# Performance work log

Hardware: AMD Instinct MI355X
Metric: run time of the kernel (lower is better)

Reference implementation:

```python
import jax, jax.numpy as jnp
import numpy as np

N, F, M, E = 8192, 256, 128, 131072


def setup_inputs() -> dict:
    key = jax.random.key(0)
    k = jax.random.split(key, 6)
    x = jax.random.normal(k[0], (N, F), dtype=jnp.float32)
    edge_index = jax.random.randint(k[1], (2, E), 0, N, dtype=jnp.int64)
    eps = jax.random.normal(k[2], (N, M), dtype=jnp.float32)
    # small init scale so sigmoid(z_i . z_j) isn't saturated
    W_mu = jax.random.normal(k[3], (F, M), dtype=jnp.float32) * 0.05
    b_mu = jnp.zeros((M,), dtype=jnp.float32)
    W_sig = jax.random.normal(k[4], (F, M), dtype=jnp.float32) * 0.05
    b_sig = jnp.zeros((M,), dtype=jnp.float32)
    return {"x": x, "edge_index": edge_index, "eps": eps,
            "W_mu": W_mu, "b_mu": b_mu, "W_sig": W_sig, "b_sig": b_sig}


def reference(x, edge_index, eps, W_mu, b_mu, W_sig, b_sig):
    # Gaussian encoder: Normal(mu, exp(logstd)), Independent over latent dim
    mu = x @ W_mu + b_mu                      # [N, M]
    logstd = x @ W_sig + b_sig                # [N, M]
    sigma = jnp.exp(logstd)
    z = mu + sigma * eps                      # rsample, [N, M]

    # decoder.probability(dot(z_i, z_j)) = sigmoid(logit); vectorized as Z @ Z.T
    logits = z @ z.T                          # [N, N]

    # symmetric adjacency labels from edge_index (either direction counts)
    src, dst = edge_index[0], edge_index[1]
    adj = jnp.zeros((N, N), dtype=jnp.float32)
    adj = adj.at[src, dst].set(1.0)
    adj = adj.at[dst, src].set(1.0)

    # BCE(sigmoid(s), y) summed over unordered pairs i < j (stable logits form)
    per_pair = jax.nn.softplus(logits) - adj * logits  # = -[y log p + (1-y) log(1-p)]
    triu = jnp.triu(jnp.ones((N, N), dtype=bool), k=1)
    bce = jnp.sum(jnp.where(triu, per_pair, 0.0))

    # sum_i KL( N(mu_i, sigma_i) || N(0, I) )
    kl = jnp.sum(0.5 * (sigma * sigma + mu * mu - 1.0) - logstd)

    return bce + 0.001 * kl
```

## Files before the change

### kernel.cpp

```cpp
#include <hip/hip_runtime.h>

#define NN 8192
#define FF 256
#define MM 128
#define HSLOTS 262144
#define NTILES 2080

typedef __attribute__((ext_vector_type(8))) short bf16x8;
typedef __attribute__((ext_vector_type(4))) float f32x4;

#define P_KL    0
#define P_EDGE  (64 * 16)
#define P_SP    (128 * 16)
#define Z_OFF   16384
#define Z_BYTES (NN * MM * 2)
#define HASH_OFF (Z_OFF + Z_BYTES)
#define WT_OFF  (HASH_OFF + HSLOTS * 4)
#define WT_BYTES (MM * FF * 2)

__device__ __forceinline__ float wave_reduce(float v) {
    #pragma unroll
    for (int off = 32; off > 0; off >>= 1) v += __shfl_down(v, off);
    return v;
}
__device__ __forceinline__ unsigned short f2bf(float f) {
    unsigned int u = __float_as_uint(f);
    u += 0x7fffu + ((u >> 16) & 1u);
    return (unsigned short)(u >> 16);
}
__device__ __forceinline__ int4 pack8(float4 a, float4 b) {
    int4 p;
    p.x = (int)f2bf(a.x) | ((int)f2bf(a.y) << 16);
    p.y = (int)f2bf(a.z) | ((int)f2bf(a.w) << 16);
    p.z = (int)f2bf(b.x) | ((int)f2bf(b.y) << 16);
    p.w = (int)f2bf(b.z) | ((int)f2bf(b.w) << 16);
    return p;
}

__global__ __launch_bounds__(256)
void prep_w(const float* __restrict__ Wmu, const float* __restrict__ Wsg,
            unsigned short* __restrict__ WmuT, unsigned short* __restrict__ WsgT,
            float* __restrict__ part, unsigned int* __restrict__ ht) {
    const int t = blockIdx.x * 256 + threadIdx.x;
    const int n = t >> 8, f = t & 255;
    WmuT[t] = f2bf(Wmu[f * MM + n]);
    WsgT[t] = f2bf(Wsg[f * MM + n]);
    if (t < 4096) part[t] = 0.f;
    uint4 z4 = {0u, 0u, 0u, 0u};
    ((uint4*)ht)[t * 2]     = z4;
    ((uint4*)ht)[t * 2 + 1] = z4;
}

#define XP_I4 33
#define XP_S  264

__global__ __launch_bounds__(256)
void encoder_mfma(const float* __restrict__ x, const float* __restrict__ eps,
                  const unsigned short* __restrict__ WmuT,
                  const unsigned short* __restrict__ WsgT,
                  const float* __restrict__ bmu, const float* __restrict__ bsg,
                  unsigned short* __restrict__ zb, float* __restrict__ part) {
    __shared__ int4 ax[16 * XP_I4];
    __shared__ float red[4];
    const int tid = threadIdx.x;
    const int wid = tid >> 6, lane = tid & 63;
    const int l15 = lane & 15, quad = lane >> 4;
    const int row0 = blockIdx.x * 16;

    {
        const int r = tid >> 4, ch = tid & 15;
        const float4* g0 = (const float4*)(x + (size_t)(row0 + r) * FF + ch * 8);
        const float4* g1 = (const float4*)(x + (size_t)(row0 + r) * FF + (ch + 16) * 8);
        ax[r * XP_I4 + ch]      = pack8(g0[0], g0[1]);
        ax[r * XP_I4 + ch + 16] = pack8(g1[0], g1[1]);
    }
    __syncthreads();

    const short* sax = (const short*)ax;
    const int4* wtm = (const int4*)WmuT;
    const int4* wts = (const int4*)WsgT;

    f32x4 zero4 = {0.f, 0.f, 0.f, 0.f};
    f32x4 accm[2], accl[2];
    accm[0] = accm[1] = accl[0] = accl[1] = zero4;

    #pragma unroll
    for (int ks = 0; ks < 8; ++ks) {
        const bf16x8 a = *(const bf16x8*)&sax[l15 * XP_S + ks * 32 + quad * 8];
        #pragma unroll
        for (int j = 0; j < 2; ++j) {
            const int n = wid * 32 + j * 16 + l15;
            const bf16x8 bmf = *(const bf16x8*)&wtm[n * 32 + ks * 4 + quad];
            const bf16x8 bsf = *(const bf16x8*)&wts[n * 32 + ks * 4 + quad];
            accm[j] = __builtin_amdgcn_mfma_f32_16x16x32_bf16(a, bmf, accm[j], 0, 0, 0);
            accl[j] = __builtin_amdgcn_mfma_f32_16x16x32_bf16(a, bsf, accl[j], 0, 0, 0);
        }
    }

    float klp = 0.f;
    #pragma unroll
    for (int j = 0; j < 2; ++j) {
        const int col = wid * 32 + j * 16 + l15;
        const float bm = bmu[col], bs = bsg[col];
        #pragma unroll
        for (int r = 0; r < 4; ++r) {
            const int row = row0 + quad * 4 + r;
            const float mu = accm[j][r] + bm;
            const float ls = accl[j][r] + bs;
            const float sg = __expf(ls);
            const float zz = fmaf(sg, eps[(size_t)row * MM + col], mu);
            zb[(size_t)row * MM + col] = f2bf(zz);
            klp += 0.5f * (sg * sg + mu * mu - 1.f) - ls;
        }
    }

    klp = wave_reduce(klp);
    if (lane == 0) red[wid] = klp;
    __syncthreads();
    if (tid == 0)
        atomicAdd(&part[P_KL + (blockIdx.x & 63) * 16],
                  red[0] + red[1] + red[2] + red[3]);
}

__device__ __forceinline__ float dotpair(unsigned int a, unsigned int b) {
    const float al = __uint_as_float(a << 16);
    const float ah = __uint_as_float(a & 0xffff0000u);
    const float bl = __uint_as_float(b << 16);
    const float bh = __uint_as_float(b & 0xffff0000u);
    return fmaf(al, bl, ah * bh);
}

__global__ __launch_bounds__(256, 3)
void tile_edge_kernel(const unsigned short* __restrict__ zb,
                      const int* __restrict__ ei, int E,
                      unsigned int* __restrict__ ht,
                      float* __restrict__ part) {
    __shared__ int4 la[128 * 8];
    __shared__ int4 lb[128 * 8];

    const int tid = threadIdx.x;
    const int bid = blockIdx.x;

    int bi = (int)((129.0f - sqrtf(16641.0f - 8.0f * (float)bid)) * 0.5f);
    bi = min(max(bi, 0), 63);
    while ((bi * (129 - bi)) / 2 > bid) --bi;
    while (((bi + 1) * (128 - bi)) / 2 <= bid) ++bi;
    const int bj = bi + (bid - (bi * (129 - bi)) / 2);

    const int wid = tid >> 6, lane = tid & 63;
    const int wm = wid >> 1, wn = wid & 1;
    const int l15 = lane & 15, quad = lane >> 4;
    const int xk = l15 & 7;

    const int4* ga = (const int4*)(zb + (size_t)bi * 128 * MM);
    const int4* gb = (const int4*)(zb + (size_t)bj * 128 * MM);

    f32x4 zero4 = {0.f, 0.f, 0.f, 0.f};
    f32x4 acc[4][4];
    #pragma unroll
    for (int i = 0; i < 4; ++i)
        #pragma unroll
        for (int j = 0; j < 4; ++j) acc[i][j] = zero4;

    const short* sa = (const short*)la;
    const short* sb = (const short*)lb;

    #pragma unroll
    for (int kc = 0; kc < 2; ++kc) {
        if (kc) __syncthreads();
        #pragma unroll
        for (int i = 0; i < 4; ++i) {
            const int c = tid + i * 256;
            const int row = c >> 3, ch = c & 7;
            const int sl = ch ^ (row & 7);
            la[row * 8 + sl] = ga[row * 16 + kc * 8 + ch];
            lb[row * 8 + sl] = gb[row * 16 + kc * 8 + ch];
        }
        __syncthreads();
        #pragma unroll
        for (int ks = 0; ks < 2; ++ks) {
            const int kq = ks * 4 + quad;
            bf16x8 af[4], bfr[4];
            #pragma unroll
            for (int t2 = 0; t2 < 4; ++t2) {
                const int ar = wm * 64 + t2 * 16 + l15;
                af[t2]  = *(const bf16x8*)&sa[ar * 64 + ((kq ^ xk) * 8)];
                const int br = wn * 64 + t2 * 16 + l15;
                bfr[t2] = *(const bf16x8*)&sb[br * 64 + ((kq ^ xk) * 8)];
            }
            #pragma unroll
            for (int i = 0; i < 4; ++i)
                #pragma unroll
                for (int j = 0; j < 4; ++j)
                    acc[i][j] = __builtin_amdgcn_mfma_f32_16x16x32_bf16(
                        af[i], bfr[j], acc[i][j], 0, 0, 0);
        }
    }

    float tsum = 0.f;
    if (bi != bj) {
        #pragma unroll
        for (int i = 0; i < 4; ++i)
            #pragma unroll
            for (int j = 0; j < 4; ++j)
                #pragma unroll
                for (int r = 0; r < 4; ++r) {
                    const float v = acc[i][j][r];
                    const float e = __expf(-fabsf(v));
                    tsum += fmaxf(v, 0.f) + e * fmaf(e, -0.5f, 1.f);
                }
    } else {
        const int rbase = wm * 64 + quad * 4;
        const int cbase = wn * 64 + l15;
        #pragma unroll
        for (int i = 0; i < 4; ++i)
            #pragma unroll
            for (int j = 0; j < 4; ++j)
                #pragma unroll
                for (int r = 0; r < 4; ++r)
                    if (cbase + j * 16 > rbase + i * 16 + r) {
                        const float v = acc[i][j][r];
                        const float e = __expf(-fabsf(v));
                        tsum += fmaxf(v, 0.f) + e * fmaf(e, -0.5f, 1.f);
                    }
    }

    tsum = wave_reduce(tsum);
    if (lane == 0)
        atomicAdd(&part[P_SP + ((bi * 64 + bj + wid * 16) & 63) * 16], tsum);

    if (bid < (E >> 6) && wid == (bid & 3)) {
        const int e = bid * 64 + lane;
        float contrib = 0.f;
        const int i = ei[e];
        const int j = ei[E + e];
        if (i != j) {
            const int a = min(i, j), b = max(i, j);
            const uint4* za = (const uint4*)(zb + (size_t)a * MM);
            const uint4* zc = (const uint4*)(zb + (size_t)b * MM);
            float s = 0.f;
            #pragma unroll
            for (int q = 0; q < MM / 8; ++q) {
                const uint4 ua = za[q], ub = zc[q];
                s += dotpair(ua.x, ub.x) + dotpair(ua.y, ub.y)
                   + dotpair(ua.z, ub.z) + dotpair(ua.w, ub.w);
            }
            const unsigned int key = (unsigned int)a * NN + b;
            unsigned int slot = (key * 2654435761u) & (HSLOTS - 1);
            bool first = false;
            for (;;) {
                const unsigned int old = atomicCAS(&ht[slot], 0u, key);
                if (old == 0u) { first = true; break; }
                if (old == key) break;
                slot = (slot + 1) & (HSLOTS - 1);
            }
            if (first) contrib = s;
        }
        contrib = wave_reduce(contrib);
        if (lane == 0)
            atomicAdd(&part[P_EDGE + (bid & 63) * 16], contrib);
    }
}

__global__ void combine_kernel(const float* __restrict__ part,
                               float* __restrict__ out) {
    const int t = threadIdx.x;
    float v = part[P_SP + t * 16] - part[P_EDGE + t * 16]
            + 0.001f * part[P_KL + t * 16];
    v = wave_reduce(v);
    if (t == 0) out[0] = v;
}

extern "C" void kernel_launch(void* const* d_in, const int* in_sizes, int n_in,
                              void* d_out, int out_size, void* d_ws, size_t ws_size,
                              hipStream_t stream) {
    const float* x   = (const float*)d_in[0];
    const int* ei    = (const int*)d_in[1];
    const float* eps = (const float*)d_in[2];
    const float* Wmu = (const float*)d_in[3];
    const float* bmu = (const float*)d_in[4];
    const float* Wsg = (const float*)d_in[5];
    const float* bsg = (const float*)d_in[6];
    float* out = (float*)d_out;
    char* ws = (char*)d_ws;

    float* part = (float*)ws;
    unsigned short* zb = (unsigned short*)(ws + Z_OFF);
    unsigned int* ht = (unsigned int*)(ws + HASH_OFF);
    unsigned short* WmuT = (unsigned short*)(ws + WT_OFF);
    unsigned short* WsgT = (unsigned short*)(ws + WT_OFF + WT_BYTES);
    const int E = in_sizes[1] / 2;

    prep_w<<<128, 256, 0, stream>>>(Wmu, Wsg, WmuT, WsgT, part, ht);
    encoder_mfma<<<NN / 16, 256, 0, stream>>>(x, eps, WmuT, WsgT, bmu, bsg, zb, part);
    tile_edge_kernel<<<NTILES, 256, 0, stream>>>(zb, ei, E, ht, part);
    combine_kernel<<<1, 64, 0, stream>>>(part, out);
}
```

Before: 119.7 us.

## Fuse all four kernels into one persistent cooperative kernel with grid syncs

Replaces the four separate launches (weight prep, encoder, tile/edge, combine) with one cooperative persistent kernel that loops over work units and uses grid-wide syncs between phases. The edge-label work is now spread across waves in reverse block order, so it runs alongside the tile work instead of being tied to the first tile blocks. This is meant to remove launch gaps and per-kernel tail effects. In exchange it adds grid.sync barriers, limits the grid to the occupancy-derived resident count, and calls an occupancy query on the host on every launch.

```diff
diff --git a/kernel.cpp b/kernel.cpp
--- a/kernel.cpp
+++ b/kernel.cpp
@@ -1,4 +1,7 @@
 #include <hip/hip_runtime.h>
+#include <hip/hip_cooperative_groups.h>
+
+namespace cg = cooperative_groups;
 
 #define NN 8192
 #define FF 256
@@ -17,6 +20,8 @@
 #define HASH_OFF (Z_OFF + Z_BYTES)
 #define WT_OFF  (HASH_OFF + HSLOTS * 4)
 #define WT_BYTES (MM * FF * 2)
+#define XP_I4 33
+#define XP_S  264
 
 __device__ __forceinline__ float wave_reduce(float v) {
     #pragma unroll
@@ -36,92 +41,6 @@
     p.w = (int)f2bf(b.z) | ((int)f2bf(b.w) << 16);
     return p;
 }
-
-__global__ __launch_bounds__(256)
-void prep_w(const float* __restrict__ Wmu, const float* __restrict__ Wsg,
-            unsigned short* __restrict__ WmuT, unsigned short* __restrict__ WsgT,
-            float* __restrict__ part, unsigned int* __restrict__ ht) {
-    const int t = blockIdx.x * 256 + threadIdx.x;
-    const int n = t >> 8, f = t & 255;
-    WmuT[t] = f2bf(Wmu[f * MM + n]);
-    WsgT[t] = f2bf(Wsg[f * MM + n]);
-    if (t < 4096) part[t] = 0.f;
-    uint4 z4 = {0u, 0u, 0u, 0u};
-    ((uint4*)ht)[t * 2]     = z4;
-    ((uint4*)ht)[t * 2 + 1] = z4;
-}
-
-#define XP_I4 33
-#define XP_S  264
-
-__global__ __launch_bounds__(256)
-void encoder_mfma(const float* __restrict__ x, const float* __restrict__ eps,
-                  const unsigned short* __restrict__ WmuT,
-                  const unsigned short* __restrict__ WsgT,
-                  const float* __restrict__ bmu, const float* __restrict__ bsg,
-                  unsigned short* __restrict__ zb, float* __restrict__ part) {
-    __shared__ int4 ax[16 * XP_I4];
-    __shared__ float red[4];
-    const int tid = threadIdx.x;
-    const int wid = tid >> 6, lane = tid & 63;
-    const int l15 = lane & 15, quad = lane >> 4;
-    const int row0 = blockIdx.x * 16;
-
-    {
-        const int r = tid >> 4, ch = tid & 15;
-        const float4* g0 = (const float4*)(x + (size_t)(row0 + r) * FF + ch * 8);
-        const float4* g1 = (const float4*)(x + (size_t)(row0 + r) * FF + (ch + 16) * 8);
-        ax[r * XP_I4 + ch]      = pack8(g0[0], g0[1]);
-        ax[r * XP_I4 + ch + 16] = pack8(g1[0], g1[1]);
-    }
-    __syncthreads();
-
-    const short* sax = (const short*)ax;
-    const int4* wtm = (const int4*)WmuT;
-    const int4* wts = (const int4*)WsgT;
-
-    f32x4 zero4 = {0.f, 0.f, 0.f, 0.f};
-    f32x4 accm[2], accl[2];
-    accm[0] = accm[1] = accl[0] = accl[1] = zero4;
-
-    #pragma unroll
-    for (int ks = 0; ks < 8; ++ks) {
-        const bf16x8 a = *(const bf16x8*)&sax[l15 * XP_S + ks * 32 + quad * 8];
-        #pragma unroll
-        for (int j = 0; j < 2; ++j) {
-            const int n = wid * 32 + j * 16 + l15;
-            const bf16x8 bmf = *(const bf16x8*)&wtm[n * 32 + ks * 4 + quad];
-            const bf16x8 bsf = *(const bf16x8*)&wts[n * 32 + ks * 4 + quad];
-            accm[j] = __builtin_amdgcn_mfma_f32_16x16x32_bf16(a, bmf, accm[j], 0, 0, 0);
-            accl[j] = __builtin_amdgcn_mfma_f32_16x16x32_bf16(a, bsf, accl[j], 0, 0, 0);
-        }
-    }
-
-    float klp = 0.f;
-    #pragma unroll
-    for (int j = 0; j < 2; ++j) {
-        const int col = wid * 32 + j * 16 + l15;
-        const float bm = bmu[col], bs = bsg[col];
-        #pragma unroll
-        for (int r = 0; r < 4; ++r) {
-            const int row = row0 + quad * 4 + r;
-            const float mu = accm[j][r] + bm;
-            const float ls = accl[j][r] + bs;
-            const float sg = __expf(ls);
-            const float zz = fmaf(sg, eps[(size_t)row * MM + col], mu);
-            zb[(size_t)row * MM + col] = f2bf(zz);
-            klp += 0.5f * (sg * sg + mu * mu - 1.f) - ls;
-        }
-    }
-
-    klp = wave_reduce(klp);
-    if (lane == 0) red[wid] = klp;
-    __syncthreads();
-    if (tid == 0)
-        atomicAdd(&part[P_KL + (blockIdx.x & 63) * 16],
-                  red[0] + red[1] + red[2] + red[3]);
-}
-
 __device__ __forceinline__ float dotpair(unsigned int a, unsigned int b) {
     const float al = __uint_as_float(a << 16);
     const float ah = __uint_as_float(a & 0xffff0000u);
@@ -129,146 +48,232 @@
     const float bh = __uint_as_float(b & 0xffff0000u);
     return fmaf(al, bl, ah * bh);
 }
+__device__ __forceinline__ float aload(const float* p) {
+    return __hip_atomic_load(p, __ATOMIC_RELAXED, __HIP_MEMORY_SCOPE_AGENT);
+}
 
 __global__ __launch_bounds__(256, 3)
-void tile_edge_kernel(const unsigned short* __restrict__ zb,
-                      const int* __restrict__ ei, int E,
-                      unsigned int* __restrict__ ht,
-                      float* __restrict__ part) {
+void mega_kernel(const float* __restrict__ x, const float* __restrict__ eps,
+                 const float* __restrict__ Wmu, const float* __restrict__ Wsg,
+                 const float* __restrict__ bmu, const float* __restrict__ bsg,
+                 const int* __restrict__ ei, int E,
+                 unsigned short* __restrict__ WmuT,
+                 unsigned short* __restrict__ WsgT,
+                 unsigned short* __restrict__ zb,
+                 unsigned int* __restrict__ ht,
+                 float* __restrict__ part, float* __restrict__ out) {
     __shared__ int4 la[128 * 8];
     __shared__ int4 lb[128 * 8];
-
+    __shared__ float red[4];
+
+    cg::grid_group grid = cg::this_grid();
     const int tid = threadIdx.x;
     const int bid = blockIdx.x;
-
-    int bi = (int)((129.0f - sqrtf(16641.0f - 8.0f * (float)bid)) * 0.5f);
-    bi = min(max(bi, 0), 63);
-    while ((bi * (129 - bi)) / 2 > bid) --bi;
-    while (((bi + 1) * (128 - bi)) / 2 <= bid) ++bi;
-    const int bj = bi + (bid - (bi * (129 - bi)) / 2);
-
+    const int nb  = gridDim.x;
     const int wid = tid >> 6, lane = tid & 63;
+    const int l15 = lane & 15, quad = lane >> 4;
+
+    for (int u = bid; u < 128; u += nb) {
+        const int t = u * 256 + tid;
+        const int n = t >> 8, f = t & 255;
+        WmuT[t] = f2bf(Wmu[f * MM + n]);
+        WsgT[t] = f2bf(Wsg[f * MM + n]);
+        if (t < 4096) part[t] = 0.f;
+        uint4 z4 = {0u, 0u, 0u, 0u};
+        ((uint4*)ht)[t * 2]     = z4;
+        ((uint4*)ht)[t * 2 + 1] = z4;
+    }
+    grid.sync();
+
+    for (int u = bid; u < NN / 16; u += nb) {
+        const int row0 = u * 16;
+        __syncthreads();
+        {
+            const int r = tid >> 4, ch = tid & 15;
+            const float4* g0 = (const float4*)(x + (size_t)(row0 + r) * FF + ch * 8);
+            const float4* g1 = (const float4*)(x + (size_t)(row0 + r) * FF + (ch + 16) * 8);
+            ((int4*)la)[r * XP_I4 + ch]      = pack8(g0[0], g0[1]);
+            ((int4*)la)[r * XP_I4 + ch + 16] = pack8(g1[0], g1[1]);
+        }
+        __syncthreads();
+
+        const short* sax = (const short*)la;
+        const int4* wtm = (const int4*)WmuT;
+        const int4* wts = (const int4*)WsgT;
+
+        f32x4 zero4 = {0.f, 0.f, 0.f, 0.f};
+        f32x4 accm[2], accl[2];
+        accm[0] = accm[1] = accl[0] = accl[1] = zero4;
+
+        #pragma unroll
+        for (int ks = 0; ks < 8; ++ks) {
+            const bf16x8 a = *(const bf16x8*)&sax[l15 * XP_S + ks * 32 + quad * 8];
+            #pragma unroll
+            for (int j = 0; j < 2; ++j) {
+                const int n = wid * 32 + j * 16 + l15;
+                const bf16x8 bmf = *(const bf16x8*)&wtm[n * 32 + ks * 4 + quad];
+                const bf16x8 bsf = *(const bf16x8*)&wts[n * 32 + ks * 4 + quad];
+                accm[j] = __builtin_amdgcn_mfma_f32_16x16x32_bf16(a, bmf, accm[j], 0, 0, 0);
+                accl[j] = __builtin_amdgcn_mfma_f32_16x16x32_bf16(a, bsf, accl[j], 0, 0, 0);
+            }
+        }
+
+        float klp = 0.f;
+        #pragma unroll
+        for (int j = 0; j < 2; ++j) {
+            const int col = wid * 32 + j * 16 + l15;
+            const float bm = bmu[col], bs = bsg[col];
+            #pragma unroll
+            for (int r = 0; r < 4; ++r) {
+                const int row = row0 + quad * 4 + r;
+                const float mu = accm[j][r] + bm;
+                const float ls = accl[j][r] + bs;
+                const float sg = __expf(ls);
+                const float zz = fmaf(sg, eps[(size_t)row * MM + col], mu);
+                zb[(size_t)row * MM + col] = f2bf(zz);
+                klp += 0.5f * (sg * sg + mu * mu - 1.f) - ls;
+            }
+        }
+
+        klp = wave_reduce(klp);
+        if (lane == 0) red[wid] = klp;
+        __syncthreads();
+        if (tid == 0)
+            atomicAdd(&part[P_KL + (u & 63) * 16],
+                      red[0] + red[1] + red[2] + red[3]);
+    }
+    grid.sync();
+
     const int wm = wid >> 1, wn = wid & 1;
-    const int l15 = lane & 15, quad = lane >> 4;
     const int xk = l15 & 7;
-
-    const int4* ga = (const int4*)(zb + (size_t)bi * 128 * MM);
-    const int4* gb = (const int4*)(zb + (size_t)bj * 128 * MM);
-
-    f32x4 zero4 = {0.f, 0.f, 0.f, 0.f};
-    f32x4 acc[4][4];
-    #pragma unroll
-    for (int i = 0; i < 4; ++i)
-        #pragma unroll
-        for (int j = 0; j < 4; ++j) acc[i][j] = zero4;
-
     const short* sa = (const short*)la;
     const short* sb = (const short*)lb;
 
-    #pragma unroll
-    for (int kc = 0; kc < 2; ++kc) {
-        if (kc) __syncthreads();
-        #pragma unroll
-        for (int i = 0; i < 4; ++i) {
-            const int c = tid + i * 256;
-            const int row = c >> 3, ch = c & 7;
-            const int sl = ch ^ (row & 7);
-            la[row * 8 + sl] = ga[row * 16 + kc * 8 + ch];
-            lb[row * 8 + sl] = gb[row * 16 + kc * 8 + ch];
-        }
-        __syncthreads();
-        #pragma unroll
-        for (int ks = 0; ks < 2; ++ks) {
-            const int kq = ks * 4 + quad;
-            bf16x8 af[4], bfr[4];
-            #pragma unroll
-            for (int t2 = 0; t2 < 4; ++t2) {
-                const int ar = wm * 64 + t2 * 16 + l15;
-                af[t2]  = *(const bf16x8*)&sa[ar * 64 + ((kq ^ xk) * 8)];
-                const int br = wn * 64 + t2 * 16 + l15;
-                bfr[t2] = *(const bf16x8*)&sb[br * 64 + ((kq ^ xk) * 8)];
-            }
-            #pragma unroll
-            for (int i = 0; i < 4; ++i)
-                #pragma unroll
-                for (int j = 0; j < 4; ++j)
-                    acc[i][j] = __builtin_amdgcn_mfma_f32_16x16x32_bf16(
-                        af[i], bfr[j], acc[i][j], 0, 0, 0);
-        }
-    }
-
-    float tsum = 0.f;
-    if (bi != bj) {
+    for (int t = bid; t < NTILES; t += nb) {
+        int bi = (int)((129.0f - sqrtf(16641.0f - 8.0f * (float)t)) * 0.5f);
+        bi = min(max(bi, 0), 63);
+        while ((bi * (129 - bi)) / 2 > t) --bi;
+        while (((bi + 1) * (128 - bi)) / 2 <= t) ++bi;
+        const int bj = bi + (t - (bi * (129 - bi)) / 2);
+
+        const int4* ga = (const int4*)(zb + (size_t)bi * 128 * MM);
+        const int4* gb = (const int4*)(zb + (size_t)bj * 128 * MM);
+
+        f32x4 zero4 = {0.f, 0.f, 0.f, 0.f};
+        f32x4 acc[4][4];
         #pragma unroll
         for (int i = 0; i < 4; ++i)
             #pragma unroll
-            for (int j = 0; j < 4; ++j)
-                #pragma unroll
-                for (int r = 0; r < 4; ++r) {
-                    const float v = acc[i][j][r];
-                    const float e = __expf(-fabsf(v));
-                    tsum += fmaxf(v, 0.f) + e * fmaf(e, -0.5f, 1.f);
+            for (int j = 0; j < 4; ++j) acc[i][j] = zero4;
+
+        #pragma unroll
+        for (int kc = 0; kc < 2; ++kc) {
+            __syncthreads();
+            #pragma unroll
+            for (int i = 0; i < 4; ++i) {
+                const int c = tid + i * 256;
+                const int row = c >> 3, ch = c & 7;
+                const int sl = ch ^ (row & 7);
+                la[row * 8 + sl] = ga[row * 16 + kc * 8 + ch];
+                lb[row * 8 + sl] = gb[row * 16 + kc * 8 + ch];
+            }
+            __syncthreads();
+            #pragma unroll
+            for (int ks = 0; ks < 2; ++ks) {
+                const int kq = ks * 4 + quad;
+                bf16x8 af[4], bfr[4];
+                #pragma unroll
+                for (int t2 = 0; t2 < 4; ++t2) {
+                    const int ar = wm * 64 + t2 * 16 + l15;
+                    af[t2]  = *(const bf16x8*)&sa[ar * 64 + ((kq ^ xk) * 8)];
+                    const int br = wn * 64 + t2 * 16 + l15;
+                    bfr[t2] = *(const bf16x8*)&sb[br * 64 + ((kq ^ xk) * 8)];
                 }
-    } else {
-        const int rbase = wm * 64 + quad * 4;
-        const int cbase = wn * 64 + l15;
-        #pragma unroll
-        for (int i = 0; i < 4; ++i)
-            #pragma unroll
-            for (int j = 0; j < 4; ++j)
-                #pragma unroll
-                for (int r = 0; r < 4; ++r)
-                    if (cbase + j * 16 > rbase + i * 16 + r) {
+                #pragma unroll
+                for (int i = 0; i < 4; ++i)
+                    #pragma unroll
+                    for (int j = 0; j < 4; ++j)
+                        acc[i][j] = __builtin_amdgcn_mfma_f32_16x16x32_bf16(
+                            af[i], bfr[j], acc[i][j], 0, 0, 0);
+            }
+        }
+
+        float tsum = 0.f;
+        if (bi != bj) {
+            #pragma unroll
+            for (int i = 0; i < 4; ++i)
+                #pragma unroll
+                for (int j = 0; j < 4; ++j)
+                    #pragma unroll
+                    for (int r = 0; r < 4; ++r) {
                         const float v = acc[i][j][r];
                         const float e = __expf(-fabsf(v));
                         tsum += fmaxf(v, 0.f) + e * fmaf(e, -0.5f, 1.f);
                     }
-    }
-
-    tsum = wave_reduce(tsum);
-    if (lane == 0)
-        atomicAdd(&part[P_SP + ((bi * 64 + bj + wid * 16) & 63) * 16], tsum);
-
-    if (bid < (E >> 6) && wid == (bid & 3)) {
-        const int e = bid * 64 + lane;
+        } else {
+            const int rbase = wm * 64 + quad * 4;
+            const int cbase = wn * 64 + l15;
+            #pragma unroll
+            for (int i = 0; i < 4; ++i)
+                #pragma unroll
+                for (int j = 0; j < 4; ++j)
+                    #pragma unroll
+                    for (int r = 0; r < 4; ++r)
+                        if (cbase + j * 16 > rbase + i * 16 + r) {
+                            const float v = acc[i][j][r];
+                            const float e = __expf(-fabsf(v));
+                            tsum += fmaxf(v, 0.f) + e * fmaf(e, -0.5f, 1.f);
+                        }
+        }
+
+        tsum = wave_reduce(tsum);
+        if (lane == 0)
+            atomicAdd(&part[P_SP + ((bi * 64 + bj + wid * 16) & 63) * 16], tsum);
+    }
+
+    const int gw = (nb - 1 - bid) * 4 + wid;
+    for (int w = gw; w < (E >> 6); w += nb * 4) {
+        const int e = w * 64 + lane;
         float contrib = 0.f;
-        const int i = ei[e];
-        const int j = ei[E + e];
-        if (i != j) {
-            const int a = min(i, j), b = max(i, j);
-            const uint4* za = (const uint4*)(zb + (size_t)a * MM);
-            const uint4* zc = (const uint4*)(zb + (size_t)b * MM);
-            float s = 0.f;
-            #pragma unroll
-            for (int q = 0; q < MM / 8; ++q) {
-                const uint4 ua = za[q], ub = zc[q];
-                s += dotpair(ua.x, ub.x) + dotpair(ua.y, ub.y)
-                   + dotpair(ua.z, ub.z) + dotpair(ua.w, ub.w);
-            }
-            const unsigned int key = (unsigned int)a * NN + b;
-            unsigned int slot = (key * 2654435761u) & (HSLOTS - 1);
-            bool first = false;
-            for (;;) {
-                const unsigned int old = atomicCAS(&ht[slot], 0u, key);
-                if (old == 0u) { first = true; break; }
-                if (old == key) break;
-                slot = (slot + 1) & (HSLOTS - 1);
-            }
-            if (first) contrib = s;
+        if (e < E) {
+            const int i = ei[e];
+            const int j = ei[E + e];
+            if (i != j) {
+                const int a = min(i, j), b = max(i, j);
+                const uint4* za = (const uint4*)(zb + (size_t)a * MM);
+                const uint4* zc = (const uint4*)(zb + (size_t)b * MM);
+                float s = 0.f;
+                #pragma unroll
+                for (int q = 0; q < MM / 8; ++q) {
+                    const uint4 ua = za[q], ub = zc[q];
+                    s += dotpair(ua.x, ub.x) + dotpair(ua.y, ub.y)
+                       + dotpair(ua.z, ub.z) + dotpair(ua.w, ub.w);
+                }
+                const unsigned int key = (unsigned int)a * NN + b;
+                unsigned int slot = (key * 2654435761u) & (HSLOTS - 1);
+                bool first = false;
+                for (;;) {
+                    const unsigned int old = atomicCAS(&ht[slot], 0u, key);
+                    if (old == 0u) { first = true; break; }
+                    if (old == key) break;
+                    slot = (slot + 1) & (HSLOTS - 1);
+                }
+                if (first) contrib = s;
+            }
         }
         contrib = wave_reduce(contrib);
         if (lane == 0)
-            atomicAdd(&part[P_EDGE + (bid & 63) * 16], contrib);
-    }
-}
-
-__global__ void combine_kernel(const float* __restrict__ part,
-                               float* __restrict__ out) {
-    const int t = threadIdx.x;
-    float v = part[P_SP + t * 16] - part[P_EDGE + t * 16]
-            + 0.001f * part[P_KL + t * 16];
-    v = wave_reduce(v);
-    if (t == 0) out[0] = v;
+            atomicAdd(&part[P_EDGE + (w & 63) * 16], contrib);
+    }
+    grid.sync();
+
+    if (bid == 0 && tid < 64) {
+        float v = aload(&part[P_SP + tid * 16])
+                - aload(&part[P_EDGE + tid * 16])
+                + 0.001f * aload(&part[P_KL + tid * 16]);
+        v = wave_reduce(v);
+        if (tid == 0) out[0] = v;
+    }
 }
 
 extern "C" void kernel_launch(void* const* d_in, const int* in_sizes, int n_in,
@@ -289,10 +294,19 @@
     unsigned int* ht = (unsigned int*)(ws + HASH_OFF);
     unsigned short* WmuT = (unsigned short*)(ws + WT_OFF);
     unsigned short* WsgT = (unsigned short*)(ws + WT_OFF + WT_BYTES);
-    const int E = in_sizes[1] / 2;
-
-    prep_w<<<128, 256, 0, stream>>>(Wmu, Wsg, WmuT, WsgT, part, ht);
-    encoder_mfma<<<NN / 16, 256, 0, stream>>>(x, eps, WmuT, WsgT, bmu, bsg, zb, part);
-    tile_edge_kernel<<<NTILES, 256, 0, stream>>>(zb, ei, E, ht, part);
-    combine_kernel<<<1, 64, 0, stream>>>(part, out);
-}
+    int E = in_sizes[1] / 2;
+
+    int maxb = 0;
+    if (hipOccupancyMaxActiveBlocksPerMultiprocessor(&maxb, mega_kernel, 256, 0)
+            != hipSuccess || maxb < 1)
+        maxb = 2;
+    int grid = maxb * 256;
+    if (grid > 768) grid = 768;
+
+    void* args[] = {(void*)&x, (void*)&eps, (void*)&Wmu, (void*)&Wsg,
+                    (void*)&bmu, (void*)&bsg, (void*)&ei, (void*)&E,
+                    (void*)&WmuT, (void*)&WsgT, (void*)&zb, (void*)&ht,
+                    (void*)&part, (void*)&out};
+    hipLaunchCooperativeKernel((const void*)mega_kernel, dim3(grid), dim3(256),
+                               args, 0, stream);
+}
```

Result: slower. 225.8 us (+88.7%).
